# Performance work log

Hardware: AMD Instinct MI355X
Metric: run time of the kernel (lower is better)

## Reference

```python
import jax, jax.numpy as jnp
import numpy as np

EMBED_DIM = 1024
N_HEADS = 16
B, L = 2, 2048


def setup_inputs() -> dict:
    key = jax.random.key(0)
    ks = jax.random.split(key, 7)
    D = EMBED_DIM
    s = 1.0 / np.sqrt(D)
    return {
        "inputs": jax.random.normal(ks[0], (B, L, D), dtype=jnp.float32),
        "rotation_params": jax.random.normal(ks[1], (D, D), dtype=jnp.float32) * s,
        "entangle_params": jax.random.uniform(ks[2], (N_HEADS,), dtype=jnp.float32, minval=0.5, maxval=1.5),
        "Wq": jax.random.normal(ks[3], (D, D), dtype=jnp.float32) * s,
        "Wk": jax.random.normal(ks[4], (D, D), dtype=jnp.float32) * s,
        "Wv": jax.random.normal(ks[5], (D, D), dtype=jnp.float32) * s,
        "Wo": jax.random.normal(ks[6], (D, D), dtype=jnp.float32) * s,
    }


def reference(inputs, rotation_params, entangle_params, Wq, Wk, Wv, Wo):
    Bq, Lq, D = inputs.shape
    H = N_HEADS
    hd = D // H
    # Linear (no bias, torch convention x @ W.T) followed by rotation matmul
    Q = (inputs @ Wq.T) @ rotation_params
    K = (inputs @ Wk.T) @ rotation_params
    V = (inputs @ Wv.T) @ rotation_params
    # split heads: (B, H, L, hd)
    Q = Q.reshape(Bq, Lq, H, hd).transpose(0, 2, 1, 3)
    K = K.reshape(Bq, Lq, H, hd).transpose(0, 2, 1, 3)
    V = V.reshape(Bq, Lq, H, hd).transpose(0, 2, 1, 3)
    scale = entangle_params.reshape(1, H, 1, 1) / jnp.sqrt(jnp.asarray(hd, dtype=inputs.dtype))
    scores = jnp.einsum("bhqd,bhkd->bhqk", Q, K) * scale
    attn = jax.nn.softmax(scores, axis=-1)  # dropout inert (eval / p=0)
    out = jnp.einsum("bhqk,bhkd->bhqd", attn, V)
    out = out.transpose(0, 2, 1, 3).reshape(Bq, Lq, D)
    return out @ Wo.T
```

## Files before the change

### kernel.cpp

```cpp
#include <hip/hip_runtime.h>
#include <cstdint>
#include <cstddef>

typedef __attribute__((ext_vector_type(8))) short  bf16x8;
typedef __attribute__((ext_vector_type(8))) _Float16 f16x8;
typedef __attribute__((ext_vector_type(4))) _Float16 f16x4;
typedef __attribute__((ext_vector_type(4))) float  f32x4;
typedef __attribute__((ext_vector_type(4))) unsigned short u16x4;
typedef __attribute__((ext_vector_type(2))) unsigned int u32x2;

#define LOG2E 1.44269504088896340736f
#define PBIAS 6.0f

__device__ __forceinline__ unsigned short f2bf(float f) {
  unsigned int u = __builtin_bit_cast(unsigned int, f);
  u += 0x7fffu + ((u >> 16) & 1u);
  return (unsigned short)(u >> 16);
}
__device__ __forceinline__ float bf2f(unsigned short s) {
  unsigned int u = ((unsigned int)s) << 16;
  return __builtin_bit_cast(float, u);
}

__device__ __forceinline__ float fast_exp2(float x) {
  return __builtin_amdgcn_exp2f(x);
}

__device__ __forceinline__ void gll16(const void* g, void* l) {
  __builtin_amdgcn_global_load_lds(
      (const __attribute__((address_space(1))) unsigned int*)g,
      (__attribute__((address_space(3))) unsigned int*)l, 16, 0, 0);
}

__global__ __launch_bounds__(256) void prep(
    const float* __restrict__ x,  unsigned short* __restrict__ xb,
    const float* __restrict__ Wo, unsigned short* __restrict__ Wob,
    const float* __restrict__ R,  const float* __restrict__ Wq,
    const float* __restrict__ Wk, const float* __restrict__ Wv,
    unsigned short* __restrict__ RT,  unsigned short* __restrict__ WqT,
    unsigned short* __restrict__ WkT, unsigned short* __restrict__ WvT) {
  int bid = blockIdx.x;
  __shared__ unsigned short s[64][68];
  if (bid < 5120) {
    const float* src = bid < 4096 ? x : Wo;
    unsigned short* dst = bid < 4096 ? xb : Wob;
    int i = (bid < 4096 ? bid : bid - 4096) * 256 + threadIdx.x;
    float4 v = ((const float4*)src)[i];
    u16x4 o;
    o[0] = f2bf(v.x); o[1] = f2bf(v.y); o[2] = f2bf(v.z); o[3] = f2bf(v.w);
    ((u16x4*)dst)[i] = o;
    return;
  }
  int t = bid - 5120;
  int z = t >> 8, tile = t & 255;
  const float* in = z == 0 ? R : (z == 1 ? Wq : (z == 2 ? Wk : Wv));
  unsigned short* out = z == 0 ? RT : (z == 1 ? WqT : (z == 2 ? WkT : WvT));
  int r0 = (tile >> 4) * 64, c0 = (tile & 15) * 64;
  int tt = threadIdx.x;
  int tr = tt >> 4, tc4 = (tt & 15) * 4;
  for (int i = 0; i < 4; ++i) {
    int r = tr + i * 16;
    float4 v = *(const float4*)(in + (size_t)(r0 + r) * 1024 + c0 + tc4);
    s[r][tc4 + 0] = f2bf(v.x); s[r][tc4 + 1] = f2bf(v.y);
    s[r][tc4 + 2] = f2bf(v.z); s[r][tc4 + 3] = f2bf(v.w);
  }
  __syncthreads();
  for (int i = 0; i < 4; ++i) {
    int oc = tr + i * 16;
    u16x4 o;
    o[0] = s[tc4 + 0][oc]; o[1] = s[tc4 + 1][oc];
    o[2] = s[tc4 + 2][oc]; o[3] = s[tc4 + 3][oc];
    *(u16x4*)(out + (size_t)(c0 + oc) * 1024 + r0 + tc4) = o;
  }
}

__global__ void tr_v(const unsigned short* __restrict__ in, unsigned short* __restrict__ out) {
  __shared__ unsigned short s[64][68];
  int t = threadIdx.x;
  int r0 = blockIdx.y * 64, c0 = blockIdx.x * 64;
  int tr = t >> 4, tc4 = (t & 15) * 4;
  for (int i = 0; i < 4; ++i) {
    int r = tr + i * 16;
    u16x4 v = *(const u16x4*)(in + (size_t)(r0 + r) * 1024 + c0 + tc4);
    s[r][tc4 + 0] = v[0]; s[r][tc4 + 1] = v[1]; s[r][tc4 + 2] = v[2]; s[r][tc4 + 3] = v[3];
  }
  __syncthreads();
  for (int i = 0; i < 4; ++i) {
    int oc = tr + i * 16;
    u16x4 o;
#pragma unroll
    for (int j = 0; j < 4; ++j) {
      _Float16 h = (_Float16)bf2f(s[tc4 + j][oc]);
      o[j] = __builtin_bit_cast(unsigned short, h);
    }
    int col = r0 + tc4;
    int c32 = col & 31;
    int pos = (col & ~31) + ((c32 >> 2) & 3) * 8 + (c32 >> 4) * 4;
    *(u16x4*)(out + (size_t)(c0 + oc) * 4096 + pos) = o;
  }
}

template <bool BF16OUT>
__global__ __launch_bounds__(256) void gemm_nt(
    const unsigned short* __restrict__ A,
    const unsigned short* __restrict__ B0, const unsigned short* __restrict__ B1,
    const unsigned short* __restrict__ B2,
    void* __restrict__ C0, void* __restrict__ C1, void* __restrict__ C2,
    int M, int N, int K) {
  const unsigned short* B = blockIdx.z == 0 ? B0 : (blockIdx.z == 1 ? B1 : B2);
  void* Cv = blockIdx.z == 0 ? C0 : (blockIdx.z == 1 ? C1 : C2);

  __shared__ unsigned short As[128 * 64];
  __shared__ unsigned short Bs[128 * 64];

  int tid = threadIdx.x, w = tid >> 6, lane = tid & 63;
  int lo = lane & 15, quad = lane >> 4;
  int m0 = blockIdx.y * 128, n0 = blockIdx.x * 128;
  int wm = (w >> 1) * 64, wn = (w & 1) * 64;

  f32x4 z4 = {0.f, 0.f, 0.f, 0.f};
  f32x4 acc[4][4];
  for (int mi = 0; mi < 4; ++mi)
    for (int ni = 0; ni < 4; ++ni) acc[mi][ni] = z4;

  int rloc = lane >> 3;
  int srcChunk = (lane & 7) ^ (rloc & 7);
  int cbase = w * 4;
  const unsigned short* Ag = A + (size_t)(m0 + cbase * 8 + rloc) * K + srcChunk * 8;
  const unsigned short* Bg = B + (size_t)(n0 + cbase * 8 + rloc) * K + srcChunk * 8;
  int ldsOfs = cbase * 512 + lane * 8;
  int cx0 = (quad ^ (lane & 7)) * 8;
  int cx1 = ((quad + 4) ^ (lane & 7)) * 8;

  for (int k0 = 0; k0 < K; k0 += 64) {
#pragma unroll
    for (int j = 0; j < 4; ++j) {
      gll16(Ag + (size_t)j * 8 * K + k0, As + ldsOfs + j * 512);
      gll16(Bg + (size_t)j * 8 * K + k0, Bs + ldsOfs + j * 512);
    }
    __syncthreads();
#pragma unroll
    for (int ks = 0; ks < 2; ++ks) {
      int cx = ks ? cx1 : cx0;
      bf16x8 af[4], bfr[4];
#pragma unroll
      for (int mi = 0; mi < 4; ++mi)
        af[mi] = *(const bf16x8*)(As + (wm + mi * 16 + lo) * 64 + cx);
#pragma unroll
      for (int ni = 0; ni < 4; ++ni)
        bfr[ni] = *(const bf16x8*)(Bs + (wn + ni * 16 + lo) * 64 + cx);
#pragma unroll
      for (int mi = 0; mi < 4; ++mi)
#pragma unroll
        for (int ni = 0; ni < 4; ++ni)
          acc[mi][ni] = __builtin_amdgcn_mfma_f32_16x16x32_bf16(af[mi], bfr[ni], acc[mi][ni], 0, 0, 0);
    }
    __syncthreads();
  }

#pragma unroll
  for (int mi = 0; mi < 4; ++mi)
#pragma unroll
    for (int ni = 0; ni < 4; ++ni)
      for (int i = 0; i < 4; ++i) {
        int r = m0 + wm + mi * 16 + quad * 4 + i;
        int c = n0 + wn + ni * 16 + lo;
        if (BF16OUT)
          ((unsigned short*)Cv)[(size_t)r * N + c] = f2bf(acc[mi][ni][i]);
        else
          ((float*)Cv)[(size_t)r * N + c] = acc[mi][ni][i];
      }
}

__global__ __launch_bounds__(256, 4) void flash_attn(
    const unsigned short* __restrict__ Q, const unsigned short* __restrict__ Kg_,
    const unsigned short* __restrict__ Vt, const float* __restrict__ ent,
    unsigned short* __restrict__ O) {
  int tid = threadIdx.x, w = tid >> 6, lane = tid & 63;
  int lo = lane & 15, quad = lane >> 4;

  int bid = blockIdx.x;
  int g = (bid & 7) + 8 * (bid >> 8);
  int qt = (bid >> 3) & 31;
  int b = g >> 4, h = g & 15;
  int q0 = qt * 64;
  float scale = ent[h] * (0.125f * LOG2E);

  __shared__ unsigned short Ks[2][64 * 64];
  __shared__ unsigned short Vts[2][64 * 64];

  bf16x8 aq[2];
#pragma unroll
  for (int ks = 0; ks < 2; ++ks) {
    uint4 v = *(const uint4*)(Q + (size_t)(b * 2048 + q0 + w * 16 + lo) * 1024 +
                              h * 64 + ks * 32 + quad * 8);
    unsigned int* pv = (unsigned int*)&v;
    uint4 o; unsigned int* po = (unsigned int*)&o;
#pragma unroll
    for (int j = 0; j < 4; ++j) {
      float f0 = bf2f((unsigned short)(pv[j] & 0xffffu)) * scale;
      float f1 = bf2f((unsigned short)(pv[j] >> 16)) * scale;
      po[j] = (unsigned int)f2bf(f0) | ((unsigned int)f2bf(f1) << 16);
    }
    aq[ks] = *(bf16x8*)&o;
  }

  f32x4 binit = {-PBIAS, -PBIAS, -PBIAS, -PBIAS};
  f32x4 z4 = {0.f, 0.f, 0.f, 0.f};
  f32x4 acco[4];
#pragma unroll
  for (int di = 0; di < 4; ++di) acco[di] = z4;
  float lsum = 0.f;

  int rloc = lane >> 3;
  int srcChunk = (lane & 7) ^ (rloc & 7);
  int cb = w * 2;
  const unsigned short* Kp = Kg_ + (size_t)(b * 2048) * 1024 + h * 64;
  const unsigned short* Vp = Vt + (size_t)(h * 64) * 4096 + (size_t)b * 2048;
  int cx0 = (quad ^ (lane & 7)) * 8;
  int cx1 = ((quad + 4) ^ (lane & 7)) * 8;

#pragma unroll
  for (int j = 0; j < 2; ++j) {
    int c = cb + j;
    int r = c * 8 + rloc;
    gll16(Kp + (size_t)r * 1024 + srcChunk * 8, Ks[0] + c * 512 + lane * 8);
    gll16(Vp + (size_t)r * 4096 + srcChunk * 8, Vts[0] + c * 512 + lane * 8);
  }

  for (int it = 0; it < 32; ++it) {
    int buf = it & 1;
    __syncthreads();
    if (it + 1 < 32) {
      int kvn = (it + 1) * 64;
#pragma unroll
      for (int j = 0; j < 2; ++j) {
        int c = cb + j;
        int r = c * 8 + rloc;
        gll16(Kp + (size_t)(kvn + r) * 1024 + srcChunk * 8, Ks[buf ^ 1] + c * 512 + lane * 8);
        gll16(Vp + (size_t)r * 4096 + kvn + srcChunk * 8, Vts[buf ^ 1] + c * 512 + lane * 8);
      }
    }
    const unsigned short* Kb_ = Ks[buf];
    const unsigned short* Vb_ = Vts[buf];

    f32x4 accs[4];
    __builtin_amdgcn_s_setprio(1);
#pragma unroll
    for (int kt = 0; kt < 4; ++kt) {
      bf16x8 kf0 = *(const bf16x8*)(Kb_ + (kt * 16 + lo) * 64 + cx0);
      bf16x8 kf1 = *(const bf16x8*)(Kb_ + (kt * 16 + lo) * 64 + cx1);
      f32x4 a = __builtin_amdgcn_mfma_f32_16x16x32_bf16(kf0, aq[0], binit, 0, 0, 0);
      accs[kt] = __builtin_amdgcn_mfma_f32_16x16x32_bf16(kf1, aq[1], a, 0, 0, 0);
    }
    __builtin_amdgcn_s_setprio(0);

    f16x4 ap[4];
#pragma unroll
    for (int kt = 0; kt < 4; ++kt) {
      float p0 = fast_exp2(accs[kt][0]);
      float p1 = fast_exp2(accs[kt][1]);
      float p2 = fast_exp2(accs[kt][2]);
      float p3 = fast_exp2(accs[kt][3]);
      lsum += (p0 + p1) + (p2 + p3);
      u32x2 uu;
      uu[0] = __builtin_bit_cast(unsigned int, __builtin_amdgcn_cvt_pkrtz(p0, p1));
      uu[1] = __builtin_bit_cast(unsigned int, __builtin_amdgcn_cvt_pkrtz(p2, p3));
      ap[kt] = __builtin_bit_cast(f16x4, uu);
    }

    __builtin_amdgcn_s_setprio(1);
#pragma unroll
    for (int t2 = 0; t2 < 2; ++t2) {
      f16x8 a8 = __builtin_shufflevector(ap[2 * t2], ap[2 * t2 + 1], 0, 1, 2, 3, 4, 5, 6, 7);
#pragma unroll
      for (int di = 0; di < 4; ++di) {
        f16x8 bv8 = *(const f16x8*)(Vb_ + (di * 16 + lo) * 64 +
                                    (((t2 * 4 + quad) ^ (lo & 7)) << 3));
        acco[di] = __builtin_amdgcn_mfma_f32_16x16x32_f16(a8, bv8, acco[di], 0, 0, 0);
      }
    }
    __builtin_amdgcn_s_setprio(0);
  }

  float v = lsum;
  v += __shfl_xor(v, 16);
  v += __shfl_xor(v, 32);
  float inv = 1.0f / v;

#pragma unroll
  for (int i = 0; i < 4; ++i) {
    float invq = __shfl(inv, quad * 4 + i);
#pragma unroll
    for (int di = 0; di < 4; ++di) {
      size_t ofs = (size_t)(b * 2048 + q0 + w * 16 + quad * 4 + i) * 1024 +
                   h * 64 + di * 16 + lo;
      O[ofs] = f2bf(acco[di][i] * invq);
    }
  }
}

extern "C" void kernel_launch(void* const* d_in, const int* in_sizes, int n_in,
                              void* d_out, int out_size, void* d_ws, size_t ws_size,
                              hipStream_t stream) {
  const float* x   = (const float*)d_in[0];
  const float* R   = (const float*)d_in[1];
  const float* ent = (const float*)d_in[2];
  const float* Wq  = (const float*)d_in[3];
  const float* Wk  = (const float*)d_in[4];
  const float* Wv  = (const float*)d_in[5];
  const float* Wo  = (const float*)d_in[6];
  float* out = (float*)d_out;

  const size_t MLD = (size_t)4096 * 1024;
  const size_t DD  = (size_t)1024 * 1024;
  if (ws_size < (MLD * 6 + DD * 8) * 2) return;

  unsigned short* ws  = (unsigned short*)d_ws;
  unsigned short* xb  = ws;
  unsigned short* RT  = xb + MLD;
  unsigned short* WqT = RT + DD;
  unsigned short* WkT = WqT + DD;
  unsigned short* WvT = WkT + DD;
  unsigned short* Wob = WvT + DD;
  unsigned short* AqT = Wob + DD;
  unsigned short* AkT = AqT + DD;
  unsigned short* AvT = AkT + DD;
  unsigned short* Qb  = AvT + DD;
  unsigned short* Kb  = Qb + MLD;
  unsigned short* Vb  = Kb + MLD;
  unsigned short* Vtf = Vb + MLD;
  unsigned short* aO  = Vtf + MLD;

  prep<<<dim3(6144), dim3(256), 0, stream>>>(
      x, xb, Wo, Wob, R, Wq, Wk, Wv, RT, WqT, WkT, WvT);

  gemm_nt<true><<<dim3(8, 8, 3), dim3(256), 0, stream>>>(
      RT, WqT, WkT, WvT, (void*)AqT, (void*)AkT, (void*)AvT, 1024, 1024, 1024);
  gemm_nt<true><<<dim3(8, 32, 3), dim3(256), 0, stream>>>(
      xb, AqT, AkT, AvT, (void*)Qb, (void*)Kb, (void*)Vb, 4096, 1024, 1024);
  tr_v<<<dim3(16, 64), dim3(256), 0, stream>>>(Vb, Vtf);
  flash_attn<<<dim3(1024), dim3(256), 0, stream>>>(Qb, Kb, Vtf, ent, aO);
  gemm_nt<false><<<dim3(8, 32, 1), dim3(256), 0, stream>>>(
      aO, Wob, Wob, Wob, (void*)out, (void*)out, (void*)out, 4096, 1024, 1024);
}
```

Baseline: 211.7 us.

## Process two 16-row Q fragments per warp in flash attention to reuse K/V tiles

Each wavefront now handles 32 query rows (two 16-row fragments) instead of 16, so a block covers 128 queries and the grid halves to 512 blocks. Each K and V fragment read from LDS now feeds twice as many MFMAs, and global K/V traffic per query is halved. In exchange register pressure roughly doubles (launch bounds lowered to 2 blocks per SIMD group), and the smaller grid of 512 blocks may underfill the GPU's 256 CUs or reduce latency hiding.

```diff
diff --git a/kernel.cpp b/kernel.cpp
--- a/kernel.cpp
+++ b/kernel.cpp
@@ -172,7 +172,7 @@
       }
 }
 
-__global__ __launch_bounds__(256, 4) void flash_attn(
+__global__ __launch_bounds__(256, 2) void flash_attn(
     const unsigned short* __restrict__ Q, const unsigned short* __restrict__ Kg_,
     const unsigned short* __restrict__ Vt, const float* __restrict__ ent,
     unsigned short* __restrict__ O) {
@@ -180,37 +180,41 @@
   int lo = lane & 15, quad = lane >> 4;
 
   int bid = blockIdx.x;
-  int g = (bid & 7) + 8 * (bid >> 8);
-  int qt = (bid >> 3) & 31;
+  int g = (bid & 7) + 8 * (bid >> 7);
+  int qt = (bid >> 3) & 15;
   int b = g >> 4, h = g & 15;
-  int q0 = qt * 64;
+  int q0 = qt * 128;
   float scale = ent[h] * (0.125f * LOG2E);
 
   __shared__ unsigned short Ks[2][64 * 64];
   __shared__ unsigned short Vts[2][64 * 64];
 
-  bf16x8 aq[2];
-#pragma unroll
-  for (int ks = 0; ks < 2; ++ks) {
-    uint4 v = *(const uint4*)(Q + (size_t)(b * 2048 + q0 + w * 16 + lo) * 1024 +
-                              h * 64 + ks * 32 + quad * 8);
-    unsigned int* pv = (unsigned int*)&v;
-    uint4 o; unsigned int* po = (unsigned int*)&o;
-#pragma unroll
-    for (int j = 0; j < 4; ++j) {
-      float f0 = bf2f((unsigned short)(pv[j] & 0xffffu)) * scale;
-      float f1 = bf2f((unsigned short)(pv[j] >> 16)) * scale;
-      po[j] = (unsigned int)f2bf(f0) | ((unsigned int)f2bf(f1) << 16);
-    }
-    aq[ks] = *(bf16x8*)&o;
-  }
+  bf16x8 aq[2][2];
+#pragma unroll
+  for (int f = 0; f < 2; ++f)
+#pragma unroll
+    for (int ks = 0; ks < 2; ++ks) {
+      uint4 v = *(const uint4*)(Q + (size_t)(b * 2048 + q0 + w * 32 + f * 16 + lo) * 1024 +
+                                h * 64 + ks * 32 + quad * 8);
+      unsigned int* pv = (unsigned int*)&v;
+      uint4 o; unsigned int* po = (unsigned int*)&o;
+#pragma unroll
+      for (int j = 0; j < 4; ++j) {
+        float f0 = bf2f((unsigned short)(pv[j] & 0xffffu)) * scale;
+        float f1 = bf2f((unsigned short)(pv[j] >> 16)) * scale;
+        po[j] = (unsigned int)f2bf(f0) | ((unsigned int)f2bf(f1) << 16);
+      }
+      aq[f][ks] = *(bf16x8*)&o;
+    }
 
   f32x4 binit = {-PBIAS, -PBIAS, -PBIAS, -PBIAS};
   f32x4 z4 = {0.f, 0.f, 0.f, 0.f};
-  f32x4 acco[4];
-#pragma unroll
-  for (int di = 0; di < 4; ++di) acco[di] = z4;
-  float lsum = 0.f;
+  f32x4 acco[4][2];
+#pragma unroll
+  for (int di = 0; di < 4; ++di) {
+    acco[di][0] = z4; acco[di][1] = z4;
+  }
+  float lsum0 = 0.f, lsum1 = 0.f;
 
   int rloc = lane >> 3;
   int srcChunk = (lane & 7) ^ (rloc & 7);
@@ -244,58 +248,70 @@
     const unsigned short* Kb_ = Ks[buf];
     const unsigned short* Vb_ = Vts[buf];
 
-    f32x4 accs[4];
+    f32x4 accs[4][2];
     __builtin_amdgcn_s_setprio(1);
 #pragma unroll
     for (int kt = 0; kt < 4; ++kt) {
       bf16x8 kf0 = *(const bf16x8*)(Kb_ + (kt * 16 + lo) * 64 + cx0);
       bf16x8 kf1 = *(const bf16x8*)(Kb_ + (kt * 16 + lo) * 64 + cx1);
-      f32x4 a = __builtin_amdgcn_mfma_f32_16x16x32_bf16(kf0, aq[0], binit, 0, 0, 0);
-      accs[kt] = __builtin_amdgcn_mfma_f32_16x16x32_bf16(kf1, aq[1], a, 0, 0, 0);
+#pragma unroll
+      for (int f = 0; f < 2; ++f) {
+        f32x4 a = __builtin_amdgcn_mfma_f32_16x16x32_bf16(kf0, aq[f][0], binit, 0, 0, 0);
+        accs[kt][f] = __builtin_amdgcn_mfma_f32_16x16x32_bf16(kf1, aq[f][1], a, 0, 0, 0);
+      }
     }
     __builtin_amdgcn_s_setprio(0);
 
-    f16x4 ap[4];
+    f16x4 ap[4][2];
 #pragma unroll
     for (int kt = 0; kt < 4; ++kt) {
-      float p0 = fast_exp2(accs[kt][0]);
-      float p1 = fast_exp2(accs[kt][1]);
-      float p2 = fast_exp2(accs[kt][2]);
-      float p3 = fast_exp2(accs[kt][3]);
-      lsum += (p0 + p1) + (p2 + p3);
-      u32x2 uu;
-      uu[0] = __builtin_bit_cast(unsigned int, __builtin_amdgcn_cvt_pkrtz(p0, p1));
-      uu[1] = __builtin_bit_cast(unsigned int, __builtin_amdgcn_cvt_pkrtz(p2, p3));
-      ap[kt] = __builtin_bit_cast(f16x4, uu);
+#pragma unroll
+      for (int f = 0; f < 2; ++f) {
+        float p0 = fast_exp2(accs[kt][f][0]);
+        float p1 = fast_exp2(accs[kt][f][1]);
+        float p2 = fast_exp2(accs[kt][f][2]);
+        float p3 = fast_exp2(accs[kt][f][3]);
+        if (f == 0) lsum0 += (p0 + p1) + (p2 + p3);
+        else        lsum1 += (p0 + p1) + (p2 + p3);
+        u32x2 uu;
+        uu[0] = __builtin_bit_cast(unsigned int, __builtin_amdgcn_cvt_pkrtz(p0, p1));
+        uu[1] = __builtin_bit_cast(unsigned int, __builtin_amdgcn_cvt_pkrtz(p2, p3));
+        ap[kt][f] = __builtin_bit_cast(f16x4, uu);
+      }
     }
 
     __builtin_amdgcn_s_setprio(1);
 #pragma unroll
     for (int t2 = 0; t2 < 2; ++t2) {
-      f16x8 a8 = __builtin_shufflevector(ap[2 * t2], ap[2 * t2 + 1], 0, 1, 2, 3, 4, 5, 6, 7);
+      f16x8 a80 = __builtin_shufflevector(ap[2 * t2][0], ap[2 * t2 + 1][0], 0, 1, 2, 3, 4, 5, 6, 7);
+      f16x8 a81 = __builtin_shufflevector(ap[2 * t2][1], ap[2 * t2 + 1][1], 0, 1, 2, 3, 4, 5, 6, 7);
 #pragma unroll
       for (int di = 0; di < 4; ++di) {
         f16x8 bv8 = *(const f16x8*)(Vb_ + (di * 16 + lo) * 64 +
                                     (((t2 * 4 + quad) ^ (lo & 7)) << 3));
-        acco[di] = __builtin_amdgcn_mfma_f32_16x16x32_f16(a8, bv8, acco[di], 0, 0, 0);
+        acco[di][0] = __builtin_amdgcn_mfma_f32_16x16x32_f16(a80, bv8, acco[di][0], 0, 0, 0);
+        acco[di][1] = __builtin_amdgcn_mfma_f32_16x16x32_f16(a81, bv8, acco[di][1], 0, 0, 0);
       }
     }
     __builtin_amdgcn_s_setprio(0);
   }
 
-  float v = lsum;
-  v += __shfl_xor(v, 16);
-  v += __shfl_xor(v, 32);
-  float inv = 1.0f / v;
-
-#pragma unroll
-  for (int i = 0; i < 4; ++i) {
-    float invq = __shfl(inv, quad * 4 + i);
-#pragma unroll
-    for (int di = 0; di < 4; ++di) {
-      size_t ofs = (size_t)(b * 2048 + q0 + w * 16 + quad * 4 + i) * 1024 +
-                   h * 64 + di * 16 + lo;
-      O[ofs] = f2bf(acco[di][i] * invq);
+#pragma unroll
+  for (int f = 0; f < 2; ++f) {
+    float v = f == 0 ? lsum0 : lsum1;
+    v += __shfl_xor(v, 16);
+    v += __shfl_xor(v, 32);
+    float inv = 1.0f / v;
+
+#pragma unroll
+    for (int i = 0; i < 4; ++i) {
+      float invq = __shfl(inv, quad * 4 + i);
+#pragma unroll
+      for (int di = 0; di < 4; ++di) {
+        size_t ofs = (size_t)(b * 2048 + q0 + w * 32 + f * 16 + quad * 4 + i) * 1024 +
+                     h * 64 + di * 16 + lo;
+        O[ofs] = f2bf(acco[di][f][i] * invq);
+      }
     }
   }
 }
@@ -340,7 +356,7 @@
   gemm_nt<true><<<dim3(8, 32, 3), dim3(256), 0, stream>>>(
       xb, AqT, AkT, AvT, (void*)Qb, (void*)Kb, (void*)Vb, 4096, 1024, 1024);
   tr_v<<<dim3(16, 64), dim3(256), 0, stream>>>(Vb, Vtf);
-  flash_attn<<<dim3(1024), dim3(256), 0, stream>>>(Qb, Kb, Vtf, ent, aO);
+  flash_attn<<<dim3(512), dim3(256), 0, stream>>>(Qb, Kb, Vtf, ent, aO);
   gemm_nt<false><<<dim3(8, 32, 1), dim3(256), 0, stream>>>(
       aO, Wob, Wob, Wob, (void*)out, (void*)out, (void*)out, 4096, 1024, 1024);
 }
```

Result: no change. 210.5 us (-0.6%).
